# Kernel optimization log

Hardware: AMD Instinct MI355X
Metric: run time of the kernel (lower is better)

The kernel has to match this reference:

```python
import jax, jax.numpy as jnp
import numpy as np
from jax import lax

BN_EPS = 1e-5


def _conv(x, w, b):
    # 3x3 conv, stride 1, padding 1 (SAME), NCHW/OIHW
    y = lax.conv_general_dilated(x, w, (1, 1), 'SAME',
                                 dimension_numbers=('NCHW', 'OIHW', 'NCHW'))
    return y + b[None, :, None, None]


def _bn(x, g, b, m, v):
    # eval-mode batchnorm with running stats
    scale = (g / jnp.sqrt(v + BN_EPS))[None, :, None, None]
    return (x - m[None, :, None, None]) * scale + b[None, :, None, None]


def _pool(x):
    # MaxPool2d(2,2), VALID (floor division of spatial dims)
    return lax.reduce_window(x, -jnp.inf, lax.max, (1, 1, 2, 2), (1, 1, 2, 2), 'VALID')


def _quantum(xq, qp):
    """Batched 5-qubit statevector sim of the PennyLane circuit.
    Wire i: RX(xq[:, i%2]) then RY(qp[i%2]); CNOT(0,1); CNOT(1,2); <Z0 Z1>.
    xq: [B, 32] (only first 2 features used). Returns [B] float32.
    """
    B = xq.shape[0]
    psi = jnp.zeros((B, 32), jnp.complex64).at[:, 0].set(1.0)
    for i in range(5):  # fixed tiny loop over wires
        a = xq[:, i % 2]          # [B] data angle
        th = qp[i % 2]            # scalar weight angle
        ca, sa = jnp.cos(a * 0.5), jnp.sin(a * 0.5)
        RX = jnp.stack([jnp.stack([ca, -1j * sa], -1),
                        jnp.stack([-1j * sa, ca], -1)], -2).astype(jnp.complex64)  # [B,2,2]
        cb, sb = jnp.cos(th * 0.5), jnp.sin(th * 0.5)
        RY = jnp.stack([jnp.stack([cb, -sb]), jnp.stack([sb, cb])]).astype(jnp.complex64)  # [2,2]
        U = jnp.einsum('ij,bjk->bik', RY, RX)  # [B,2,2] per-wire unitary
        psi = psi.reshape(B, 2 ** i, 2, 2 ** (4 - i))
        psi = jnp.einsum('bij,bajc->baic', U, psi).reshape(B, 32)
    psi = psi.reshape(B, 2, 2, 2, 2, 2)
    # CNOT(0,1): flip qubit 1 where qubit 0 == 1
    psi = psi.at[:, 1].set(psi[:, 1, ::-1])
    # CNOT(1,2): flip qubit 2 where qubit 1 == 1
    psi = psi.at[:, :, 1].set(psi[:, :, 1, ::-1])
    z01 = jnp.array([[1.0, -1.0], [-1.0, 1.0]], jnp.float32).reshape(1, 2, 2, 1, 1, 1)
    prob = jnp.real(psi) ** 2 + jnp.imag(psi) ** 2
    return jnp.sum(prob * z01, axis=(1, 2, 3, 4, 5))


def setup_inputs() -> dict:
    key = jax.random.key(0)
    ks = jax.random.split(key, 24)
    B = 8192
    s = 0.05
    d = {}
    d['x'] = jax.random.normal(ks[0], (B, 1, 28, 28), jnp.float32)
    d['conv1_w'] = jax.random.normal(ks[1], (64, 1, 3, 3), jnp.float32) * s
    d['conv1_b'] = jax.random.normal(ks[2], (64,), jnp.float32) * s
    d['conv2_w'] = jax.random.normal(ks[3], (128, 64, 3, 3), jnp.float32) * s
    d['conv2_b'] = jax.random.normal(ks[4], (128,), jnp.float32) * s
    d['conv3_w'] = jax.random.normal(ks[5], (256, 128, 3, 3), jnp.float32) * s
    d['conv3_b'] = jax.random.normal(ks[6], (256,), jnp.float32) * s
    for i, c in [(1, 64), (2, 128), (3, 256)]:
        d[f'bn{i}_g'] = jnp.ones((c,), jnp.float32)
        d[f'bn{i}_b'] = jnp.zeros((c,), jnp.float32)
        d[f'bn{i}_m'] = jax.random.normal(ks[6 + i], (c,), jnp.float32) * 0.1
        d[f'bn{i}_v'] = jax.random.uniform(ks[9 + i], (c,), jnp.float32, 0.5, 1.5)
    d['fc1_w'] = jax.random.normal(ks[13], (32, 256 * 3 * 3), jnp.float32) * s
    d['fc1_b'] = jax.random.normal(ks[14], (32,), jnp.float32) * s
    d['q_params'] = jax.random.uniform(ks[15], (8,), jnp.float32)
    d['fc2_w'] = jax.random.normal(ks[16], (128, 1), jnp.float32) * s
    d['fc2_b'] = jax.random.normal(ks[17], (128,), jnp.float32) * s
    d['fc3_w'] = jax.random.normal(ks[18], (2, 128), jnp.float32) * s
    d['fc3_b'] = jax.random.normal(ks[19], (2,), jnp.float32) * s
    return d


def reference(x, conv1_w, conv1_b, conv2_w, conv2_b, conv3_w, conv3_b,
              bn1_g, bn1_b, bn1_m, bn1_v, bn2_g, bn2_b, bn2_m, bn2_v,
              bn3_g, bn3_b, bn3_m, bn3_v, fc1_w, fc1_b, q_params,
              fc2_w, fc2_b, fc3_w, fc3_b):
    h = _pool(jax.nn.relu(_bn(_conv(x, conv1_w, conv1_b), bn1_g, bn1_b, bn1_m, bn1_v)))
    h = _pool(jax.nn.relu(_bn(_conv(h, conv2_w, conv2_b), bn2_g, bn2_b, bn2_m, bn2_v)))
    h = _pool(jax.nn.relu(_bn(_conv(h, conv3_w, conv3_b), bn3_g, bn3_b, bn3_m, bn3_v)))
    # dropout is identity in eval mode
    h = h.reshape(h.shape[0], -1)              # [B, 2304]
    h = h @ fc1_w.T + fc1_b                     # [B, 32]
    q = _quantum(h, q_params)[:, None]          # [B, 1]
    h = q @ fc2_w.T + fc2_b                     # [B, 128]
    logits = h @ fc3_w.T + fc3_b                # [B, 2]
    return jax.nn.log_softmax(logits, axis=1)
```

## Files before the change

### kernel.cpp

```cpp
#include <hip/hip_runtime.h>
#include <hip/hip_bf16.h>
#include <math.h>

typedef float f32x4 __attribute__((ext_vector_type(4)));
typedef short s16x8 __attribute__((ext_vector_type(8)));
typedef float v2f   __attribute__((ext_vector_type(2)));

static const long long OFF_W2  = 0LL;
static const long long OFF_W3  = 147456LL;
static const long long OFF_AB1 = 737280LL;
static const long long OFF_AB2 = 737792LL;
static const long long OFF_AB3 = 738816LL;
static const long long OFF_Q   = 740864LL;

__device__ inline unsigned short f2bfu(float f) {
    __hip_bfloat16 h = __float2bfloat16(f);
    unsigned short u;
    __builtin_memcpy(&u, &h, 2);
    return u;
}

__global__ __launch_bounds__(256) void prep_k(
    const float* __restrict__ c2w, const float* __restrict__ c3w,
    const float* __restrict__ c1b, const float* __restrict__ g1, const float* __restrict__ b1,
    const float* __restrict__ m1, const float* __restrict__ v1,
    const float* __restrict__ c2b, const float* __restrict__ g2, const float* __restrict__ b2,
    const float* __restrict__ m2, const float* __restrict__ v2,
    const float* __restrict__ c3b, const float* __restrict__ g3, const float* __restrict__ b3,
    const float* __restrict__ m3, const float* __restrict__ v3,
    const float* __restrict__ fc1b, const float* __restrict__ qp,
    const float* __restrict__ fc2w, const float* __restrict__ fc2b,
    const float* __restrict__ fc3w, const float* __restrict__ fc3b,
    short* __restrict__ wT2, short* __restrict__ wT3,
    float2* __restrict__ ab1, float2* __restrict__ ab2, float2* __restrict__ ab3,
    float* __restrict__ qc)
{
    int tid = blockIdx.x * 256 + threadIdx.x;
    if (tid < 73728) {
        int ic = tid & 63, oc = (tid >> 6) & 127, k = tid >> 13;
        wT2[tid] = (short)f2bfu(c2w[(oc * 64 + ic) * 9 + k]);
    }
    if (tid < 294912) {
        int ic = tid & 127, oc = (tid >> 7) & 255, k = tid >> 15;
        wT3[tid] = (short)f2bfu(c3w[(oc * 128 + ic) * 9 + k]);
    }
    if (tid < 64) {
        float s = g1[tid] / sqrtf(v1[tid] + 1e-5f);
        ab1[tid] = make_float2(s, (c1b[tid] - m1[tid]) * s + b1[tid]);
    } else if (tid < 192) {
        int c = tid - 64;
        float s = g2[c] / sqrtf(v2[c] + 1e-5f);
        ab2[c] = make_float2(s, (c2b[c] - m2[c]) * s + b2[c]);
    } else if (tid < 448) {
        int c = tid - 192;
        float s = g3[c] / sqrtf(v3[c] + 1e-5f);
        ab3[c] = make_float2(s, (c3b[c] - m3[c]) * s + b3[c]);
    } else if (tid == 448) {
        float A0 = 0.f, A1 = 0.f, B0 = 0.f, B1 = 0.f;
        for (int k = 0; k < 128; ++k) {
            float f2 = fc2w[k], fb = fc2b[k];
            A0 += fc3w[k] * f2;        B0 += fc3w[k] * fb;
            A1 += fc3w[128 + k] * f2;  B1 += fc3w[128 + k] * fb;
        }
        qc[0] = A0; qc[1] = A1;
        qc[2] = B0 + fc3b[0]; qc[3] = B1 + fc3b[1];
        qc[4] = cosf(qp[1]);  qc[5] = fc1b[1];
    }
}

__global__ __launch_bounds__(256, 2) void fused_k(
    const float* __restrict__ x, const float* __restrict__ c1w,
    const float2* __restrict__ ab1, const float2* __restrict__ ab2,
    const float2* __restrict__ ab3,
    const short* __restrict__ wT2, const short* __restrict__ wT3,
    const float* __restrict__ fc1w, const float* __restrict__ qc,
    float* __restrict__ out)
{
    __shared__ short smem[16 * 16 * 64 + 128];
    __shared__ float xt[30][32];
    __shared__ float red[4];

    int b = blockIdx.x, t = threadIdx.x;

    for (int i = t; i < 8256; i += 256) ((unsigned*)smem)[i] = 0u;
    for (int i = t; i < 960;  i += 256) ((float*)xt)[i] = 0.f;
    __syncthreads();

    for (int i = t; i < 784; i += 256) xt[i / 28 + 1][i % 28 + 1] = x[b * 784 + i];
    __syncthreads();

    int ocg = t & 7;
    int posb = t >> 3;
#pragma unroll 1
    for (int pass = 0; pass < 2; ++pass) {
        int oc0 = ocg * 8 + pass * 4;
        float wr[4][9];
        float2 abr[4];
#pragma unroll
        for (int c = 0; c < 4; ++c) {
#pragma unroll
            for (int k = 0; k < 9; ++k) wr[c][k] = c1w[(oc0 + c) * 9 + k];
            abr[c] = ab1[oc0 + c];
        }
        for (int p = posb; p < 196; p += 32) {
            int py = p / 14, px = p % 14;
            int y0 = 2 * py, x0 = 2 * px;
            v2f rowv[4][2];
#pragma unroll
            for (int i = 0; i < 4; ++i) {
                rowv[i][0] = *(const v2f*)&xt[y0 + i][x0];
                rowv[i][1] = *(const v2f*)&xt[y0 + i][x0 + 2];
            }
            unsigned short ub[4];
#pragma unroll
            for (int c = 0; c < 4; ++c) {
                v2f a0 = {0.f, 0.f}, a1 = {0.f, 0.f};
#pragma unroll
                for (int ky = 0; ky < 3; ++ky) {
                    float w0 = wr[c][ky * 3 + 0], w1 = wr[c][ky * 3 + 1], w2 = wr[c][ky * 3 + 2];
                    v2f p00 = rowv[ky][0],     p01 = rowv[ky][1];
                    v2f p10 = rowv[ky + 1][0], p11 = rowv[ky + 1][1];
                    v2f q0; q0.x = p00.y; q0.y = p01.x;
                    v2f q1; q1.x = p10.y; q1.y = p11.x;
                    a0 += p00 * w0; a0 += q0 * w1; a0 += p01 * w2;
                    a1 += p10 * w0; a1 += q1 * w1; a1 += p11 * w2;
                }
                float aa = abr[c].x, bb = abr[c].y;
                v2f r0 = a0 * aa + bb;
                v2f r1 = a1 * aa + bb;
                float v = fmaxf(fmaxf(fmaxf(r0.x, r0.y), fmaxf(r1.x, r1.y)), 0.f);
                ub[c] = f2bfu(v);
            }
            uint2 pk;
            pk.x = (unsigned)ub[0] | ((unsigned)ub[1] << 16);
            pk.y = (unsigned)ub[2] | ((unsigned)ub[3] << 16);
            int blk = ocg ^ ((px + 1) & 7);
            *(uint2*)&smem[((((py + 1) * 16) + (px + 1)) * 8 + blk) * 8 + pass * 4] = pk;
        }
    }
    __syncthreads();

    int lane = t & 63, wid = t >> 6;
    int quad = lane >> 4, n16 = lane & 15;
    int dy = n16 >> 3, lx = n16 & 7;
    int cb = wid >> 1;
    int oh = wid & 1;

    {
        f32x4 acc[4][7];
        f32x4 z = {0.f, 0.f, 0.f, 0.f};
#pragma unroll
        for (int ml = 0; ml < 4; ++ml)
#pragma unroll
            for (int ry = 0; ry < 7; ++ry) acc[ml][ry] = z;

#pragma unroll 1
        for (int kykx = 0; kykx < 9; ++kykx) {
            int ky = kykx / 3, kx = kykx - 3 * ky;
            int y0 = dy + ky;
            int xc = lx + kx + cb * 8;
            const short* aB = wT2 + (kykx * 128 + oh * 64 + n16) * 64 + quad * 8;
#pragma unroll
            for (int kk = 0; kk < 2; ++kk) {
                int blk = (kk * 4 + quad) ^ (xc & 7);
                const short* bp = &smem[((y0 * 16 + xc) * 8 + blk) * 8];
                s16x8 A[4];
#pragma unroll
                for (int ml = 0; ml < 4; ++ml)
                    A[ml] = *(const s16x8*)(aB + ml * 1024 + kk * 32);
#pragma unroll
                for (int ry = 0; ry < 7; ++ry) {
                    s16x8 B = *(const s16x8*)(bp + ry * 2048);
#pragma unroll
                    for (int ml = 0; ml < 4; ++ml)
                        acc[ml][ry] = __builtin_amdgcn_mfma_f32_16x16x32_bf16(A[ml], B, acc[ml][ry], 0, 0, 0);
                }
            }
        }

        __syncthreads();
        for (int i = t; i < 4224; i += 256) ((unsigned*)smem)[i] = 0u;
        __syncthreads();

        int m = lx >> 1;
        int xp = cb * 4 + m;
        bool keep = (dy == 0) && ((lx & 1) == 0) && (xp < 7);
#pragma unroll
        for (int ml = 0; ml < 4; ++ml) {
            int oc0 = oh * 64 + ml * 16 + quad * 4;
            float2 abv[4];
#pragma unroll
            for (int r = 0; r < 4; ++r) abv[r] = ab2[oc0 + r];
#pragma unroll
            for (int ry = 0; ry < 7; ++ry) {
                float pv[4];
#pragma unroll
                for (int r = 0; r < 4; ++r) {
                    float v = acc[ml][ry][r] * abv[r].x + abv[r].y;
                    v = fmaxf(v, __shfl_xor(v, 1));
                    v = fmaxf(v, __shfl_xor(v, 8));
                    pv[r] = fmaxf(v, 0.f);
                }
                if (keep) {
                    uint2 pk;
                    pk.x = (unsigned)f2bfu(pv[0]) | ((unsigned)f2bfu(pv[1]) << 16);
                    pk.y = (unsigned)f2bfu(pv[2]) | ((unsigned)f2bfu(pv[3]) << 16);
                    int blk3 = (oc0 >> 3) ^ (((xp + 1) & 7) << 1);
                    *(uint2*)&smem[(((ry + 1) * 8 + (xp + 1)) * 16 + blk3) * 8 + (oc0 & 7)] = pk;
                }
            }
        }
    }
    __syncthreads();

    int oq = wid;

    f32x4 acc3[4][3];
    {
        f32x4 z = {0.f, 0.f, 0.f, 0.f};
#pragma unroll
        for (int ml = 0; ml < 4; ++ml)
#pragma unroll
            for (int nt = 0; nt < 3; ++nt) acc3[ml][nt] = z;
    }

#pragma unroll 1
    for (int kykx = 0; kykx < 9; ++kykx) {
        int ky = kykx / 3, kx = kykx - 3 * ky;
        int y0 = dy + ky;
        int x0 = lx + kx;
        const short* aB = wT3 + (kykx * 256 + oq * 64 + n16) * 128 + quad * 8;
#pragma unroll
        for (int kk = 0; kk < 4; ++kk) {
            int blk = (kk * 4 + quad) ^ ((x0 & 7) << 1);
            const short* bp = &smem[((y0 * 8 + x0) * 16 + blk) * 8];
            s16x8 B0 = *(const s16x8*)(bp);
            s16x8 B1 = *(const s16x8*)(bp + 2048);
            s16x8 B2 = *(const s16x8*)(bp + 4096);
#pragma unroll
            for (int ml = 0; ml < 4; ++ml) {
                s16x8 A = *(const s16x8*)(aB + ml * 2048 + kk * 32);
                acc3[ml][0] = __builtin_amdgcn_mfma_f32_16x16x32_bf16(A, B0, acc3[ml][0], 0, 0, 0);
                acc3[ml][1] = __builtin_amdgcn_mfma_f32_16x16x32_bf16(A, B1, acc3[ml][1], 0, 0, 0);
                acc3[ml][2] = __builtin_amdgcn_mfma_f32_16x16x32_bf16(A, B2, acc3[ml][2], 0, 0, 0);
            }
        }
    }

    float vacc = 0.f;
    {
        int m = lx >> 1;
        bool keep = (dy == 0) && ((lx & 1) == 0) && (m < 3);
        const float* fc1w1 = fc1w + 2304;
#pragma unroll
        for (int ml = 0; ml < 4; ++ml) {
            int oc0 = oq * 64 + ml * 16 + quad * 4;
            float2 abv[4];
#pragma unroll
            for (int r = 0; r < 4; ++r) abv[r] = ab3[oc0 + r];
#pragma unroll
            for (int nt = 0; nt < 3; ++nt) {
#pragma unroll
                for (int r = 0; r < 4; ++r) {
                    float v = acc3[ml][nt][r] * abv[r].x + abv[r].y;
                    v = fmaxf(v, __shfl_xor(v, 1));
                    v = fmaxf(v, __shfl_xor(v, 8));
                    v = fmaxf(v, 0.f);
                    if (keep) vacc += v * fc1w1[(oc0 + r) * 9 + nt * 3 + m];
                }
            }
        }
    }
#pragma unroll
    for (int s = 1; s < 64; s <<= 1) vacc += __shfl_xor(vacc, s);
    if (lane == 0) red[wid] = vacc;
    __syncthreads();
    if (t == 0) {
        float v = red[0] + red[1] + red[2] + red[3] + qc[5];
        float q = cosf(v) * qc[4];
        float l0 = q * qc[0] + qc[2];
        float l1 = q * qc[1] + qc[3];
        float mx = fmaxf(l0, l1);
        float lse = mx + logf(__expf(l0 - mx) + __expf(l1 - mx));
        out[b * 2 + 0] = l0 - lse;
        out[b * 2 + 1] = l1 - lse;
    }
}

extern "C" void kernel_launch(void* const* d_in, const int* in_sizes, int n_in,
                              void* d_out, int out_size, void* d_ws, size_t ws_size,
                              hipStream_t stream)
{
    const float* x    = (const float*)d_in[0];
    const float* c1w  = (const float*)d_in[1];
    const float* c1b  = (const float*)d_in[2];
    const float* c2w  = (const float*)d_in[3];
    const float* c2b  = (const float*)d_in[4];
    const float* c3w  = (const float*)d_in[5];
    const float* c3b  = (const float*)d_in[6];
    const float* g1   = (const float*)d_in[7];
    const float* b1   = (const float*)d_in[8];
    const float* m1   = (const float*)d_in[9];
    const float* v1   = (const float*)d_in[10];
    const float* g2   = (const float*)d_in[11];
    const float* b2   = (const float*)d_in[12];
    const float* m2   = (const float*)d_in[13];
    const float* v2   = (const float*)d_in[14];
    const float* g3   = (const float*)d_in[15];
    const float* b3   = (const float*)d_in[16];
    const float* m3   = (const float*)d_in[17];
    const float* v3   = (const float*)d_in[18];
    const float* fc1w = (const float*)d_in[19];
    const float* fc1b = (const float*)d_in[20];
    const float* qp   = (const float*)d_in[21];
    const float* fc2w = (const float*)d_in[22];
    const float* fc2b = (const float*)d_in[23];
    const float* fc3w = (const float*)d_in[24];
    const float* fc3b = (const float*)d_in[25];
    float* out = (float*)d_out;
    char* ws = (char*)d_ws;

    short*  wT2 = (short*)(ws + OFF_W2);
    short*  wT3 = (short*)(ws + OFF_W3);
    float2* ab1 = (float2*)(ws + OFF_AB1);
    float2* ab2 = (float2*)(ws + OFF_AB2);
    float2* ab3 = (float2*)(ws + OFF_AB3);
    float*  qc  = (float*)(ws + OFF_Q);

    int B = in_sizes[0] / 784;

    prep_k<<<1152, 256, 0, stream>>>(c2w, c3w, c1b, g1, b1, m1, v1,
                                     c2b, g2, b2, m2, v2, c3b, g3, b3, m3, v3,
                                     fc1b, qp, fc2w, fc2b, fc3w, fc3b,
                                     wT2, wT3, ab1, ab2, ab3, qc);
    fused_k<<<B, 256, 0, stream>>>(x, c1w, ab1, ab2, ab3, wT2, wT3, fc1w, qc, out);
}
```

Baseline: 1.040 ms.

## Prefetch MFMA weight fragments one step ahead and split LDS buffers for conv3

The conv2 and conv3 MFMA loops are flattened into single loops over (tap, k-chunk), and the next step's weight fragments are loaded from global memory into registers while the current MFMAs run. This hides global-load latency behind compute. The conv3 input moves to its own LDS buffer, zeroed at startup, which removes a barrier/zero/barrier sequence between conv2 and its epilogue but raises LDS use per block. Conv1 is restructured into one pass with 16 channel groups, and bf16 packing now uses the paired conversion intrinsic. The extra prefetch registers and LDS could reduce occupancy under launch_bounds(256,2).

```diff
diff --git a/kernel.cpp b/kernel.cpp
--- a/kernel.cpp
+++ b/kernel.cpp
@@ -17,6 +17,13 @@
     __hip_bfloat16 h = __float2bfloat16(f);
     unsigned short u;
     __builtin_memcpy(&u, &h, 2);
+    return u;
+}
+
+__device__ inline unsigned pack2bf(float a, float b) {
+    __hip_bfloat162 h = __float22bfloat162_rn(make_float2(a, b));
+    unsigned u;
+    __builtin_memcpy(&u, &h, 4);
     return u;
 }
 
@@ -76,67 +83,66 @@
     const float* __restrict__ fc1w, const float* __restrict__ qc,
     float* __restrict__ out)
 {
-    __shared__ short smem[16 * 16 * 64 + 128];
+    __shared__ short smem2[16 * 16 * 64 + 128];
+    __shared__ short xs3[8 * 8 * 128 + 256];
     __shared__ float xt[30][32];
     __shared__ float red[4];
 
     int b = blockIdx.x, t = threadIdx.x;
 
-    for (int i = t; i < 8256; i += 256) ((unsigned*)smem)[i] = 0u;
+    for (int i = t; i < 8256; i += 256) ((unsigned*)smem2)[i] = 0u;
+    for (int i = t; i < 4224; i += 256) ((unsigned*)xs3)[i] = 0u;
     for (int i = t; i < 960;  i += 256) ((float*)xt)[i] = 0.f;
     __syncthreads();
 
     for (int i = t; i < 784; i += 256) xt[i / 28 + 1][i % 28 + 1] = x[b * 784 + i];
-    __syncthreads();
-
-    int ocg = t & 7;
-    int posb = t >> 3;
-#pragma unroll 1
-    for (int pass = 0; pass < 2; ++pass) {
-        int oc0 = ocg * 8 + pass * 4;
-        float wr[4][9];
-        float2 abr[4];
+
+    int og4 = t & 15;
+    int oc0a = og4 * 4;
+    float wr[4][9];
+    float2 abr[4];
+#pragma unroll
+    for (int c = 0; c < 4; ++c) {
+#pragma unroll
+        for (int k = 0; k < 9; ++k) wr[c][k] = c1w[(oc0a + c) * 9 + k];
+        abr[c] = ab1[oc0a + c];
+    }
+    __syncthreads();
+
+    int posb = t >> 4;
+    for (int p = posb; p < 196; p += 16) {
+        int py = p / 14, px = p % 14;
+        int y0 = 2 * py, x0 = 2 * px;
+        v2f rowv[4][2];
+#pragma unroll
+        for (int i = 0; i < 4; ++i) {
+            rowv[i][0] = *(const v2f*)&xt[y0 + i][x0];
+            rowv[i][1] = *(const v2f*)&xt[y0 + i][x0 + 2];
+        }
+        float pv[4];
 #pragma unroll
         for (int c = 0; c < 4; ++c) {
-#pragma unroll
-            for (int k = 0; k < 9; ++k) wr[c][k] = c1w[(oc0 + c) * 9 + k];
-            abr[c] = ab1[oc0 + c];
-        }
-        for (int p = posb; p < 196; p += 32) {
-            int py = p / 14, px = p % 14;
-            int y0 = 2 * py, x0 = 2 * px;
-            v2f rowv[4][2];
-#pragma unroll
-            for (int i = 0; i < 4; ++i) {
-                rowv[i][0] = *(const v2f*)&xt[y0 + i][x0];
-                rowv[i][1] = *(const v2f*)&xt[y0 + i][x0 + 2];
-            }
-            unsigned short ub[4];
-#pragma unroll
-            for (int c = 0; c < 4; ++c) {
-                v2f a0 = {0.f, 0.f}, a1 = {0.f, 0.f};
-#pragma unroll
-                for (int ky = 0; ky < 3; ++ky) {
-                    float w0 = wr[c][ky * 3 + 0], w1 = wr[c][ky * 3 + 1], w2 = wr[c][ky * 3 + 2];
-                    v2f p00 = rowv[ky][0],     p01 = rowv[ky][1];
-                    v2f p10 = rowv[ky + 1][0], p11 = rowv[ky + 1][1];
-                    v2f q0; q0.x = p00.y; q0.y = p01.x;
-                    v2f q1; q1.x = p10.y; q1.y = p11.x;
-                    a0 += p00 * w0; a0 += q0 * w1; a0 += p01 * w2;
-                    a1 += p10 * w0; a1 += q1 * w1; a1 += p11 * w2;
-                }
-                float aa = abr[c].x, bb = abr[c].y;
-                v2f r0 = a0 * aa + bb;
-                v2f r1 = a1 * aa + bb;
-                float v = fmaxf(fmaxf(fmaxf(r0.x, r0.y), fmaxf(r1.x, r1.y)), 0.f);
-                ub[c] = f2bfu(v);
-            }
-            uint2 pk;
-            pk.x = (unsigned)ub[0] | ((unsigned)ub[1] << 16);
-            pk.y = (unsigned)ub[2] | ((unsigned)ub[3] << 16);
-            int blk = ocg ^ ((px + 1) & 7);
-            *(uint2*)&smem[((((py + 1) * 16) + (px + 1)) * 8 + blk) * 8 + pass * 4] = pk;
-        }
+            v2f a0 = {0.f, 0.f}, a1 = {0.f, 0.f};
+#pragma unroll
+            for (int ky = 0; ky < 3; ++ky) {
+                float w0 = wr[c][ky * 3 + 0], w1 = wr[c][ky * 3 + 1], w2 = wr[c][ky * 3 + 2];
+                v2f p00 = rowv[ky][0],     p01 = rowv[ky][1];
+                v2f p10 = rowv[ky + 1][0], p11 = rowv[ky + 1][1];
+                v2f q0; q0.x = p00.y; q0.y = p01.x;
+                v2f q1; q1.x = p10.y; q1.y = p11.x;
+                a0 += p00 * w0; a0 += q0 * w1; a0 += p01 * w2;
+                a1 += p10 * w0; a1 += q1 * w1; a1 += p11 * w2;
+            }
+            float aa = abr[c].x, bb = abr[c].y;
+            v2f r0 = a0 * aa + bb;
+            v2f r1 = a1 * aa + bb;
+            pv[c] = fmaxf(fmaxf(fmaxf(r0.x, r0.y), fmaxf(r1.x, r1.y)), 0.f);
+        }
+        uint2 pk;
+        pk.x = pack2bf(pv[0], pv[1]);
+        pk.y = pack2bf(pv[2], pv[3]);
+        int blk = (og4 >> 1) ^ ((px + 1) & 7);
+        *(uint2*)&smem2[((((py + 1) * 16) + (px + 1)) * 8 + blk) * 8 + (og4 & 1) * 4] = pk;
     }
     __syncthreads();
 
@@ -154,33 +160,33 @@
 #pragma unroll
             for (int ry = 0; ry < 7; ++ry) acc[ml][ry] = z;
 
+        const short* aB0 = wT2 + oh * 4096 + n16 * 64 + quad * 8;
+        s16x8 Ac[4], An[4];
+#pragma unroll
+        for (int ml = 0; ml < 4; ++ml) Ac[ml] = *(const s16x8*)(aB0 + ml * 1024);
+
 #pragma unroll 1
-        for (int kykx = 0; kykx < 9; ++kykx) {
+        for (int it = 0; it < 18; ++it) {
+            int kykx = it >> 1, kk = it & 1;
             int ky = kykx / 3, kx = kykx - 3 * ky;
             int y0 = dy + ky;
             int xc = lx + kx + cb * 8;
-            const short* aB = wT2 + (kykx * 128 + oh * 64 + n16) * 64 + quad * 8;
-#pragma unroll
-            for (int kk = 0; kk < 2; ++kk) {
-                int blk = (kk * 4 + quad) ^ (xc & 7);
-                const short* bp = &smem[((y0 * 16 + xc) * 8 + blk) * 8];
-                s16x8 A[4];
+            int blk = (kk * 4 + quad) ^ (xc & 7);
+            const short* bp = &smem2[((y0 * 16 + xc) * 8 + blk) * 8];
+            int itn = (it < 17) ? it + 1 : 0;
+            const short* an = aB0 + (itn >> 1) * 8192 + (itn & 1) * 32;
+#pragma unroll
+            for (int ml = 0; ml < 4; ++ml) An[ml] = *(const s16x8*)(an + ml * 1024);
+#pragma unroll
+            for (int ry = 0; ry < 7; ++ry) {
+                s16x8 B = *(const s16x8*)(bp + ry * 2048);
 #pragma unroll
                 for (int ml = 0; ml < 4; ++ml)
-                    A[ml] = *(const s16x8*)(aB + ml * 1024 + kk * 32);
-#pragma unroll
-                for (int ry = 0; ry < 7; ++ry) {
-                    s16x8 B = *(const s16x8*)(bp + ry * 2048);
-#pragma unroll
-                    for (int ml = 0; ml < 4; ++ml)
-                        acc[ml][ry] = __builtin_amdgcn_mfma_f32_16x16x32_bf16(A[ml], B, acc[ml][ry], 0, 0, 0);
-                }
-            }
-        }
-
-        __syncthreads();
-        for (int i = t; i < 4224; i += 256) ((unsigned*)smem)[i] = 0u;
-        __syncthreads();
+                    acc[ml][ry] = __builtin_amdgcn_mfma_f32_16x16x32_bf16(Ac[ml], B, acc[ml][ry], 0, 0, 0);
+            }
+#pragma unroll
+            for (int ml = 0; ml < 4; ++ml) Ac[ml] = An[ml];
+        }
 
         int m = lx >> 1;
         int xp = cb * 4 + m;
@@ -203,10 +209,10 @@
                 }
                 if (keep) {
                     uint2 pk;
-                    pk.x = (unsigned)f2bfu(pv[0]) | ((unsigned)f2bfu(pv[1]) << 16);
-                    pk.y = (unsigned)f2bfu(pv[2]) | ((unsigned)f2bfu(pv[3]) << 16);
+                    pk.x = pack2bf(pv[0], pv[1]);
+                    pk.y = pack2bf(pv[2], pv[3]);
                     int blk3 = (oc0 >> 3) ^ (((xp + 1) & 7) << 1);
-                    *(uint2*)&smem[(((ry + 1) * 8 + (xp + 1)) * 16 + blk3) * 8 + (oc0 & 7)] = pk;
+                    *(uint2*)&xs3[(((ry + 1) * 8 + (xp + 1)) * 16 + blk3) * 8 + (oc0 & 7)] = pk;
                 }
             }
         }
@@ -224,26 +230,35 @@
             for (int nt = 0; nt < 3; ++nt) acc3[ml][nt] = z;
     }
 
+    {
+        const short* aC0 = wT3 + oq * 8192 + n16 * 128 + quad * 8;
+        s16x8 Ac[4], An[4];
+#pragma unroll
+        for (int ml = 0; ml < 4; ++ml) Ac[ml] = *(const s16x8*)(aC0 + ml * 2048);
+
 #pragma unroll 1
-    for (int kykx = 0; kykx < 9; ++kykx) {
-        int ky = kykx / 3, kx = kykx - 3 * ky;
-        int y0 = dy + ky;
-        int x0 = lx + kx;
-        const short* aB = wT3 + (kykx * 256 + oq * 64 + n16) * 128 + quad * 8;
-#pragma unroll
-        for (int kk = 0; kk < 4; ++kk) {
+        for (int it = 0; it < 36; ++it) {
+            int kykx = it >> 2, kk = it & 3;
+            int ky = kykx / 3, kx = kykx - 3 * ky;
+            int y0 = dy + ky;
+            int x0 = lx + kx;
             int blk = (kk * 4 + quad) ^ ((x0 & 7) << 1);
-            const short* bp = &smem[((y0 * 8 + x0) * 16 + blk) * 8];
+            const short* bp = &xs3[((y0 * 8 + x0) * 16 + blk) * 8];
+            int itn = (it < 35) ? it + 1 : 0;
+            const short* an = aC0 + (itn >> 2) * 32768 + (itn & 3) * 32;
+#pragma unroll
+            for (int ml = 0; ml < 4; ++ml) An[ml] = *(const s16x8*)(an + ml * 2048);
             s16x8 B0 = *(const s16x8*)(bp);
             s16x8 B1 = *(const s16x8*)(bp + 2048);
             s16x8 B2 = *(const s16x8*)(bp + 4096);
 #pragma unroll
             for (int ml = 0; ml < 4; ++ml) {
-                s16x8 A = *(const s16x8*)(aB + ml * 2048 + kk * 32);
-                acc3[ml][0] = __builtin_amdgcn_mfma_f32_16x16x32_bf16(A, B0, acc3[ml][0], 0, 0, 0);
-                acc3[ml][1] = __builtin_amdgcn_mfma_f32_16x16x32_bf16(A, B1, acc3[ml][1], 0, 0, 0);
-                acc3[ml][2] = __builtin_amdgcn_mfma_f32_16x16x32_bf16(A, B2, acc3[ml][2], 0, 0, 0);
-            }
+                acc3[ml][0] = __builtin_amdgcn_mfma_f32_16x16x32_bf16(Ac[ml], B0, acc3[ml][0], 0, 0, 0);
+                acc3[ml][1] = __builtin_amdgcn_mfma_f32_16x16x32_bf16(Ac[ml], B1, acc3[ml][1], 0, 0, 0);
+                acc3[ml][2] = __builtin_amdgcn_mfma_f32_16x16x32_bf16(Ac[ml], B2, acc3[ml][2], 0, 0, 0);
+            }
+#pragma unroll
+            for (int ml = 0; ml < 4; ++ml) Ac[ml] = An[ml];
         }
     }
 
```

Result: slower. 1.063 ms (+2.3%).
